# Kernel tuning notes

Hardware: AMD Instinct MI355X
Metric: run time of the kernel (lower is better)

Reference implementation:

```python
import jax, jax.numpy as jnp
import numpy as np

N_HEADS = 16


def setup_inputs() -> dict:
    key = jax.random.key(0)
    k1, k2, k3, k4, k5 = jax.random.split(key, 5)
    B, T, C = 2, 2048, 1024
    x = jax.random.normal(k1, (B, T, C), dtype=jnp.float32)
    rotary_cos_sin = jax.random.normal(k2, (T, C // N_HEADS), dtype=jnp.float32)  # unused by forward
    c = jax.random.normal(k3, (B, C), dtype=jnp.float32)  # unused by forward
    # Linear weights, torch convention: y = x @ W.T
    W_qkv = jax.random.normal(k4, (3 * C, C), dtype=jnp.float32) * (1.0 / np.sqrt(C))
    W_out = jax.random.normal(k5, (C, C), dtype=jnp.float32) * (1.0 / np.sqrt(C))
    return {"x": x, "rotary_cos_sin": rotary_cos_sin, "c": c, "W_qkv": W_qkv, "W_out": W_out}


def reference(x, rotary_cos_sin, c, W_qkv, W_out):
    B, T, C = x.shape
    H = N_HEADS
    D = C // H
    # qkv projection (no bias)
    qkv = jnp.einsum('btc,fc->btf', x, W_qkv)          # [B,T,3C]
    q, k, v = jnp.split(qkv, 3, axis=-1)
    q = q.reshape(B, T, H, D)
    k = k.reshape(B, T, H, D)
    v = v.reshape(B, T, H, D)
    # manual attention: full TxT score matrix, as in the original
    att = jnp.einsum('bthd,bshd->bhts', q, k) * (1.0 / jnp.sqrt(jnp.asarray(D, x.dtype)))
    att = jax.nn.softmax(att, axis=-1)
    # attn_dropout / resid_dropout are identity at inference
    y = jnp.einsum('bhts,bshd->bthd', att, v).reshape(B, T, C)
    return jnp.einsum('btc,oc->bto', y, W_out)
```

## Files before the change

kernel.cpp:

```cpp
#include <hip/hip_runtime.h>
#include <hip/hip_bf16.h>

typedef __bf16 bf16;
typedef __attribute__((ext_vector_type(4))) __bf16 bf16x4;
typedef __attribute__((ext_vector_type(8))) __bf16 bf16x8;
typedef __attribute__((ext_vector_type(4))) float f32x4;
typedef __attribute__((ext_vector_type(16))) float f32x16;

#define MFMA16(A, B, C) __builtin_amdgcn_mfma_f32_16x16x32_bf16((A), (B), (C), 0, 0, 0)
#define MFMA32(A, B, C) __builtin_amdgcn_mfma_f32_32x32x16_bf16((A), (B), (C), 0, 0, 0)

union U8 { unsigned w[4]; bf16x8 v; };

__device__ __forceinline__ void gload_lds16(const void* g, void* l) {
    __builtin_amdgcn_global_load_lds(
        (const __attribute__((address_space(1))) void*)g,
        (__attribute__((address_space(3))) void*)l,
        16, 0, 0);
}

__device__ __forceinline__ unsigned pk2(float a, float b) {
    union { bf16 h[2]; unsigned u; } t;
    t.h[0] = (bf16)a; t.h[1] = (bf16)b;
    return t.u;
}

__device__ __forceinline__ unsigned long long tr16(unsigned addr) {
    unsigned long long r;
    asm volatile("ds_read_b64_tr_b16 %0, %1" : "=v"(r) : "v"(addr));
    return r;
}

__global__ __launch_bounds__(256) void cast_f32_bf16(
    const float* __restrict__ in, bf16* __restrict__ out)
{
    const int i = (blockIdx.x * 256 + threadIdx.x) * 8;
    const float4 a = *(const float4*)(in + i);
    const float4 b = *(const float4*)(in + i + 4);
    bf16x8 o;
    o[0] = (bf16)a.x; o[1] = (bf16)a.y; o[2] = (bf16)a.z; o[3] = (bf16)a.w;
    o[4] = (bf16)b.x; o[5] = (bf16)b.y; o[6] = (bf16)b.z; o[7] = (bf16)b.w;
    *(bf16x8*)(out + i) = o;
}

template <typename OutT>
__global__ __launch_bounds__(256) void gemm_bt128(
    const bf16* __restrict__ A, const bf16* __restrict__ B, OutT* __restrict__ C,
    int M, int N, int K)
{
    constexpr int BK = 32;
    __shared__ __align__(16) bf16 sA[128 * BK];
    __shared__ __align__(16) bf16 sB[128 * BK];

    const int tid  = threadIdx.x;
    const int lane = tid & 63;
    const int wave = tid >> 6;
    const int wr   = wave >> 1;
    const int wc   = wave & 1;
    const int bm   = blockIdx.y * 128;
    const int bn   = blockIdx.x * 128;

    f32x4 acc[4][4] = {};

    const size_t ldb = (size_t)K * 2;
    const int srow = wave * 32 + (lane >> 2);
    const int scol = (lane & 3) * 16;
    const char* Ab = (const char*)A + (size_t)(bm + srow) * ldb + scol;
    const char* Bb = (const char*)B + (size_t)(bn + srow) * ldb + scol;
    char* ldsA = (char*)sA + wave * 2048;
    char* ldsB = (char*)sB + wave * 2048;

    const int arow = wr * 64 + (lane & 15);
    const int brow = wc * 64 + (lane & 15);
    const int koff = (lane >> 4) * 8;

    for (int k0 = 0; k0 < K; k0 += BK) {
        __syncthreads();
        const size_t kb = (size_t)k0 * 2;
        gload_lds16(Ab + kb,            ldsA);
        gload_lds16(Ab + kb + 16 * ldb, ldsA + 1024);
        gload_lds16(Bb + kb,            ldsB);
        gload_lds16(Bb + kb + 16 * ldb, ldsB + 1024);
        __syncthreads();

        bf16x8 af[4], bfr[4];
#pragma unroll
        for (int m = 0; m < 4; ++m)
            af[m] = *(const bf16x8*)&sA[(arow + m * 16) * BK + koff];
#pragma unroll
        for (int n = 0; n < 4; ++n)
            bfr[n] = *(const bf16x8*)&sB[(brow + n * 16) * BK + koff];
#pragma unroll
        for (int m = 0; m < 4; ++m)
#pragma unroll
            for (int n = 0; n < 4; ++n)
                acc[m][n] = MFMA16(af[m], bfr[n], acc[m][n]);
    }

    const int crow0 = bm + wr * 64 + (lane >> 4) * 4;
    const int ccol0 = bn + wc * 64 + (lane & 15);
#pragma unroll
    for (int m = 0; m < 4; ++m)
#pragma unroll
        for (int n = 0; n < 4; ++n)
#pragma unroll
            for (int j = 0; j < 4; ++j)
                C[(size_t)(crow0 + m * 16 + j) * N + ccol0 + n * 16] = (OutT)acc[m][n][j];
}

__global__ __launch_bounds__(512, 4) void attn32(
    const bf16* __restrict__ qkv, bf16* __restrict__ y)
{
    constexpr int T = 2048, F = 3072, Cd = 1024;
    constexpr float c1 = 0.18033688011112042f;

    __shared__ __align__(16) char smem[38912];

    const int tid = threadIdx.x, lane = tid & 63, w = tid >> 6;
    const int wq = w & 3, grp = w >> 2;
    const int hi = lane >> 5, q5 = lane & 31;
    const int bh = blockIdx.y, b = bh >> 4, h = bh & 15;
    const bf16* qkvb = qkv + (size_t)b * T * F;
    const int qcol = h * 64, kcol = Cd + h * 64, vcol = 2 * Cd + h * 64;

    char* sKg = smem + grp * 8192;
    char* sVg = smem + 16384 + grp * 8192;

    const int gq = blockIdx.x * 128 + wq * 32 + q5;
    bf16x8 qf[4];
#pragma unroll
    for (int s = 0; s < 4; ++s)
        qf[s] = *(const bf16x8*)(qkvb + (size_t)gq * F + qcol + s * 16 + hi * 8);

    const int ck0 = (wq * 2 + 0) * 64 + lane, ck1 = ck0 + 64;
    const int kvk0 = ck0 >> 3, d0k0 = ((ck0 & 7) ^ (kvk0 & 7)) << 3;
    const int kvk1 = ck1 >> 3, d0k1 = ((ck1 & 7) ^ (kvk1 & 7)) << 3;
    const int cv0 = ck0, cv1 = ck1;
    const int kvv0 = ((cv0 >> 1) & 3) | (((cv0 >> 5) & 1) << 2) | (((cv0 >> 4) & 1) << 3) | (((cv0 >> 6) & 3) << 4);
    const int dv0  = ((cv0 & 1) << 3) | (((cv0 >> 3) & 1) << 4) | (((cv0 >> 8) & 1) << 5);
    const int kvv1 = ((cv1 >> 1) & 3) | (((cv1 >> 5) & 1) << 2) | (((cv1 >> 4) & 1) << 3) | (((cv1 >> 6) & 3) << 4);
    const int dv1  = ((cv1 & 1) << 3) | (((cv1 >> 3) & 1) << 4) | (((cv1 >> 8) & 1) << 5);

    const size_t gbase = (size_t)grp * 1024 * F * 2;
    const char* kq0 = (const char*)qkvb + gbase + (size_t)(kvk0 * F + kcol + d0k0) * 2;
    const char* kq1 = (const char*)qkvb + gbase + (size_t)(kvk1 * F + kcol + d0k1) * 2;
    const char* vq0 = (const char*)qkvb + gbase + (size_t)(kvv0 * F + vcol + dv0) * 2;
    const char* vq1 = (const char*)qkvb + gbase + (size_t)(kvv1 * F + vcol + dv1) * 2;
    char* dstK0 = sKg + (wq * 2 + 0) * 1024;
    char* dstK1 = sKg + (wq * 2 + 1) * 1024;
    char* dstV0 = sVg + (wq * 2 + 0) * 1024;
    char* dstV1 = sVg + (wq * 2 + 1) * 1024;

    const unsigned sVoff = (unsigned)(uintptr_t)(__attribute__((address_space(3))) char*)(void*)sVg;
    const unsigned trb = sVoff + 8u * (unsigned)lane;
    const unsigned swz = (unsigned)(q5 & 7) << 4;

    f32x16 oacc[2] = {};
    float m_run = -3e38f, l_run = 0.f;

    for (int it = 0; it < 16; ++it) {
        __syncthreads();
        const size_t sb = (size_t)it * 64 * F * 2;
        gload_lds16(kq0 + sb, dstK0);
        gload_lds16(kq1 + sb, dstK1);
        gload_lds16(vq0 + sb, dstV0);
        gload_lds16(vq1 + sb, dstV1);
        __syncthreads();

        f32x16 sacc[2];
        __builtin_amdgcn_s_setprio(1);
#pragma unroll
        for (int a = 0; a < 2; ++a) {
            f32x16 acc = {};
#pragma unroll
            for (int dsl = 0; dsl < 4; ++dsl) {
                const unsigned cbyte = ((unsigned)(dsl * 32 + hi * 16)) ^ swz;
                bf16x8 kf = *(const bf16x8*)(sKg + (a * 32 + q5) * 128 + cbyte);
                acc = MFMA32(kf, qf[dsl], acc);
            }
            sacc[a] = acc;
        }
        __builtin_amdgcn_s_setprio(0);

        float mt = -3e38f;
#pragma unroll
        for (int a = 0; a < 2; ++a)
#pragma unroll
            for (int r = 0; r < 16; ++r) mt = fmaxf(mt, sacc[a][r]);
        mt = fmaxf(mt, __shfl_xor(mt, 32));
        if (__any(mt > m_run + 64.0f)) {
            const float mn = fmaxf(m_run, mt);
            const float al = __builtin_exp2f((m_run - mn) * c1);
            m_run = mn;
            l_run *= al;
#pragma unroll
            for (int d = 0; d < 2; ++d)
#pragma unroll
                for (int r = 0; r < 16; ++r) oacc[d][r] *= al;
        }
        const float mc = m_run * c1;

        float rs = 0.f;
        unsigned W[2][4][2];
#pragma unroll
        for (int a = 0; a < 2; ++a)
#pragma unroll
            for (int bb = 0; bb < 4; ++bb) {
                const float p0 = __builtin_exp2f(fmaf(sacc[a][4 * bb + 0], c1, -mc));
                const float p1 = __builtin_exp2f(fmaf(sacc[a][4 * bb + 1], c1, -mc));
                const float p2 = __builtin_exp2f(fmaf(sacc[a][4 * bb + 2], c1, -mc));
                const float p3 = __builtin_exp2f(fmaf(sacc[a][4 * bb + 3], c1, -mc));
                rs += (p0 + p1) + (p2 + p3);
                W[a][bb][0] = pk2(p0, p1);
                W[a][bb][1] = pk2(p2, p3);
            }
        l_run += rs;

        unsigned Zz[2][2][2];
#pragma unroll
        for (int a = 0; a < 2; ++a)
#pragma unroll
            for (int c = 0; c < 2; ++c)
#pragma unroll
                for (int ww = 0; ww < 2; ++ww) {
                    const unsigned yv = hi ? W[a][2 * c][ww] : W[a][2 * c + 1][ww];
                    Zz[a][c][ww] = (unsigned)__shfl_xor((int)yv, 32);
                }
        bf16x8 pb[4];
#pragma unroll
        for (int a = 0; a < 2; ++a)
#pragma unroll
            for (int c = 0; c < 2; ++c) {
                U8 u;
                u.w[0] = hi ? Zz[a][c][0] : W[a][2 * c][0];
                u.w[1] = hi ? Zz[a][c][1] : W[a][2 * c][1];
                u.w[2] = hi ? W[a][2 * c + 1][0] : Zz[a][c][0];
                u.w[3] = hi ? W[a][2 * c + 1][1] : Zz[a][c][1];
                pb[2 * a + c] = u.v;
            }

        unsigned long long t0[8], t1[8];
#pragma unroll
        for (int ks = 0; ks < 4; ++ks) {
            t0[2 * ks + 0] = tr16(trb + (unsigned)(ks * 1024));
            t0[2 * ks + 1] = tr16(trb + (unsigned)(ks * 1024 + 512));
        }
#pragma unroll
        for (int ks = 0; ks < 4; ++ks) {
            t1[2 * ks + 0] = tr16(trb + (unsigned)(4096 + ks * 1024));
            t1[2 * ks + 1] = tr16(trb + (unsigned)(4096 + ks * 1024 + 512));
        }
        asm volatile("s_waitcnt lgkmcnt(8)" ::: "memory");
        __builtin_amdgcn_sched_barrier(0);
        __builtin_amdgcn_s_setprio(1);
#pragma unroll
        for (int ks = 0; ks < 4; ++ks) {
            U8 u;
            u.w[0] = (unsigned)t0[2 * ks];     u.w[1] = (unsigned)(t0[2 * ks] >> 32);
            u.w[2] = (unsigned)t0[2 * ks + 1]; u.w[3] = (unsigned)(t0[2 * ks + 1] >> 32);
            oacc[0] = MFMA32(u.v, pb[ks], oacc[0]);
        }
        __builtin_amdgcn_s_setprio(0);
        asm volatile("s_waitcnt lgkmcnt(0)" ::: "memory");
        __builtin_amdgcn_sched_barrier(0);
        __builtin_amdgcn_s_setprio(1);
#pragma unroll
        for (int ks = 0; ks < 4; ++ks) {
            U8 u;
            u.w[0] = (unsigned)t1[2 * ks];     u.w[1] = (unsigned)(t1[2 * ks] >> 32);
            u.w[2] = (unsigned)t1[2 * ks + 1]; u.w[3] = (unsigned)(t1[2 * ks + 1] >> 32);
            oacc[1] = MFMA32(u.v, pb[ks], oacc[1]);
        }
        __builtin_amdgcn_s_setprio(0);
    }

    __syncthreads();
    float* Obuf  = (float*)smem;
    float* mlbuf = (float*)(smem + 36864);
    if (grp == 1) {
        float* po = Obuf + (wq * 64 + lane) * 36;
#pragma unroll
        for (int d5 = 0; d5 < 2; ++d5)
#pragma unroll
            for (int j = 0; j < 4; ++j) {
                f32x4 t;
                t[0] = oacc[d5][4 * j + 0]; t[1] = oacc[d5][4 * j + 1];
                t[2] = oacc[d5][4 * j + 2]; t[3] = oacc[d5][4 * j + 3];
                *(f32x4*)(po + d5 * 16 + 4 * j) = t;
            }
        mlbuf[(wq * 64 + lane) * 2 + 0] = m_run;
        mlbuf[(wq * 64 + lane) * 2 + 1] = l_run;
    }
    __syncthreads();
    if (grp == 0) {
        const float mB = mlbuf[(wq * 64 + lane) * 2 + 0];
        const float lB = mlbuf[(wq * 64 + lane) * 2 + 1];
        const float m  = fmaxf(m_run, mB);
        const float fA = __builtin_exp2f((m_run - m) * c1);
        const float fB = __builtin_exp2f((mB - m) * c1);
        const float lh = l_run * fA + lB * fB;
        const float lt = lh + __shfl_xor(lh, 32);
        const float inv = 1.f / lt;
        const float* po = Obuf + (wq * 64 + lane) * 36;
        bf16* yrow = y + (size_t)(b * T + gq) * Cd + h * 64;
#pragma unroll
        for (int d5 = 0; d5 < 2; ++d5)
#pragma unroll
            for (int bb = 0; bb < 4; ++bb) {
                const f32x4 ob = *(const f32x4*)(po + d5 * 16 + 4 * bb);
                bf16x4 o4;
#pragma unroll
                for (int jj = 0; jj < 4; ++jj)
                    o4[jj] = (bf16)((oacc[d5][4 * bb + jj] * fA + ob[jj] * fB) * inv);
                *(bf16x4*)(yrow + d5 * 32 + 8 * bb + 4 * hi) = o4;
            }
    }
}

extern "C" void kernel_launch(void* const* d_in, const int* in_sizes, int n_in,
                              void* d_out, int out_size, void* d_ws, size_t ws_size,
                              hipStream_t stream) {
    (void)in_sizes; (void)n_in; (void)out_size; (void)ws_size;
    const float* x    = (const float*)d_in[0];
    const float* Wqkv = (const float*)d_in[3];
    const float* Wout = (const float*)d_in[4];
    float* out = (float*)d_out;

    bf16* xb    = (bf16*)d_ws;
    bf16* wqkvb = xb    + (size_t)4096 * 1024;
    bf16* woutb = wqkvb + (size_t)3072 * 1024;
    bf16* qkv   = woutb + (size_t)1024 * 1024;
    bf16* yb    = qkv   + (size_t)4096 * 3072;

    cast_f32_bf16<<<4096 * 1024 / 2048, 256, 0, stream>>>(x, xb);
    cast_f32_bf16<<<3072 * 1024 / 2048, 256, 0, stream>>>(Wqkv, wqkvb);
    cast_f32_bf16<<<1024 * 1024 / 2048, 256, 0, stream>>>(Wout, woutb);

    gemm_bt128<bf16><<<dim3(3072 / 128, 4096 / 128), 256, 0, stream>>>(xb, wqkvb, qkv, 4096, 3072, 1024);
    attn32<<<dim3(2048 / 128, 2 * 16), 512, 0, stream>>>(qkv, yb);
    gemm_bt128<float><<<dim3(1024 / 128, 4096 / 128), 256, 0, stream>>>(yb, woutb, out, 4096, 1024, 1024);
}
```

Baseline: 226.4 us.

## Double-buffer K/V tiles in attention, fuse casts, narrow output GEMM tile

The attention kernel now double-buffers its K/V LDS tiles, issuing the next tile's global-to-LDS loads before computing on the current one. This removes the second barrier per iteration and is meant to hide load latency. The three f32-to-bf16 cast launches become one kernel, and the output projection GEMM uses 128x64 tiles so twice as many blocks run on a grid of only 256. LDS per attention block rises to 64KB, which may lower occupancy below the launch-bounds target.

```diff
diff --git a/kernel.cpp b/kernel.cpp
--- a/kernel.cpp
+++ b/kernel.cpp
@@ -31,26 +31,33 @@
     return r;
 }
 
-__global__ __launch_bounds__(256) void cast_f32_bf16(
-    const float* __restrict__ in, bf16* __restrict__ out)
+__global__ __launch_bounds__(256) void cast3_f32_bf16(
+    const float* __restrict__ x, const float* __restrict__ wq,
+    const float* __restrict__ wo, bf16* __restrict__ out)
 {
     const int i = (blockIdx.x * 256 + threadIdx.x) * 8;
-    const float4 a = *(const float4*)(in + i);
-    const float4 b = *(const float4*)(in + i + 4);
+    const float* src;
+    int off;
+    if (i < 4194304)      { src = x;  off = i; }
+    else if (i < 7340032) { src = wq; off = i - 4194304; }
+    else                  { src = wo; off = i - 7340032; }
+    const float4 a = *(const float4*)(src + off);
+    const float4 b = *(const float4*)(src + off + 4);
     bf16x8 o;
     o[0] = (bf16)a.x; o[1] = (bf16)a.y; o[2] = (bf16)a.z; o[3] = (bf16)a.w;
     o[4] = (bf16)b.x; o[5] = (bf16)b.y; o[6] = (bf16)b.z; o[7] = (bf16)b.w;
     *(bf16x8*)(out + i) = o;
 }
 
-template <typename OutT>
-__global__ __launch_bounds__(256) void gemm_bt128(
+template <typename OutT, int BN>
+__global__ __launch_bounds__(256) void gemm_bt(
     const bf16* __restrict__ A, const bf16* __restrict__ B, OutT* __restrict__ C,
     int M, int N, int K)
 {
     constexpr int BK = 32;
+    constexpr int NF = BN / 32;
     __shared__ __align__(16) bf16 sA[128 * BK];
-    __shared__ __align__(16) bf16 sB[128 * BK];
+    __shared__ __align__(16) bf16 sB[BN * BK];
 
     const int tid  = threadIdx.x;
     const int lane = tid & 63;
@@ -58,20 +65,28 @@
     const int wr   = wave >> 1;
     const int wc   = wave & 1;
     const int bm   = blockIdx.y * 128;
-    const int bn   = blockIdx.x * 128;
-
-    f32x4 acc[4][4] = {};
+    const int bn   = blockIdx.x * BN;
+
+    f32x4 acc[4][NF] = {};
 
     const size_t ldb = (size_t)K * 2;
-    const int srow = wave * 32 + (lane >> 2);
-    const int scol = (lane & 3) * 16;
-    const char* Ab = (const char*)A + (size_t)(bm + srow) * ldb + scol;
-    const char* Bb = (const char*)B + (size_t)(bn + srow) * ldb + scol;
+    const int srowA = wave * 32 + (lane >> 2);
+    const int scolA = (lane & 3) * 16;
+    const char* Ab = (const char*)A + (size_t)(bm + srowA) * ldb + scolA;
     char* ldsA = (char*)sA + wave * 2048;
-    char* ldsB = (char*)sB + wave * 2048;
+
+    const char* Bb;
+    char* ldsB;
+    if constexpr (BN == 128) {
+        Bb   = (const char*)B + (size_t)(bn + srowA) * ldb + scolA;
+        ldsB = (char*)sB + wave * 2048;
+    } else {
+        Bb   = (const char*)B + (size_t)(bn + (tid >> 2)) * ldb + (tid & 3) * 16;
+        ldsB = (char*)sB + tid * 16;
+    }
 
     const int arow = wr * 64 + (lane & 15);
-    const int brow = wc * 64 + (lane & 15);
+    const int brow = wc * (BN / 2) + (lane & 15);
     const int koff = (lane >> 4) * 8;
 
     for (int k0 = 0; k0 < K; k0 += BK) {
@@ -79,30 +94,34 @@
         const size_t kb = (size_t)k0 * 2;
         gload_lds16(Ab + kb,            ldsA);
         gload_lds16(Ab + kb + 16 * ldb, ldsA + 1024);
-        gload_lds16(Bb + kb,            ldsB);
-        gload_lds16(Bb + kb + 16 * ldb, ldsB + 1024);
+        if constexpr (BN == 128) {
+            gload_lds16(Bb + kb,            ldsB);
+            gload_lds16(Bb + kb + 16 * ldb, ldsB + 1024);
+        } else {
+            gload_lds16(Bb + kb, ldsB);
+        }
         __syncthreads();
 
-        bf16x8 af[4], bfr[4];
+        bf16x8 af[4], bfr[NF];
 #pragma unroll
         for (int m = 0; m < 4; ++m)
             af[m] = *(const bf16x8*)&sA[(arow + m * 16) * BK + koff];
 #pragma unroll
-        for (int n = 0; n < 4; ++n)
+        for (int n = 0; n < NF; ++n)
             bfr[n] = *(const bf16x8*)&sB[(brow + n * 16) * BK + koff];
 #pragma unroll
         for (int m = 0; m < 4; ++m)
 #pragma unroll
-            for (int n = 0; n < 4; ++n)
+            for (int n = 0; n < NF; ++n)
                 acc[m][n] = MFMA16(af[m], bfr[n], acc[m][n]);
     }
 
     const int crow0 = bm + wr * 64 + (lane >> 4) * 4;
-    const int ccol0 = bn + wc * 64 + (lane & 15);
+    const int ccol0 = bn + wc * (BN / 2) + (lane & 15);
 #pragma unroll
     for (int m = 0; m < 4; ++m)
 #pragma unroll
-        for (int n = 0; n < 4; ++n)
+        for (int n = 0; n < NF; ++n)
 #pragma unroll
             for (int j = 0; j < 4; ++j)
                 C[(size_t)(crow0 + m * 16 + j) * N + ccol0 + n * 16] = (OutT)acc[m][n][j];
@@ -114,7 +133,7 @@
     constexpr int T = 2048, F = 3072, Cd = 1024;
     constexpr float c1 = 0.18033688011112042f;
 
-    __shared__ __align__(16) char smem[38912];
+    __shared__ __align__(16) char smem[65536];
 
     const int tid = threadIdx.x, lane = tid & 63, w = tid >> 6;
     const int wq = w & 3, grp = w >> 2;
@@ -123,8 +142,7 @@
     const bf16* qkvb = qkv + (size_t)b * T * F;
     const int qcol = h * 64, kcol = Cd + h * 64, vcol = 2 * Cd + h * 64;
 
-    char* sKg = smem + grp * 8192;
-    char* sVg = smem + 16384 + grp * 8192;
+    const int grpbase = grp * 32768;
 
     const int gq = blockIdx.x * 128 + wq * 32 + q5;
     bf16x8 qf[4];
@@ -146,26 +164,39 @@
     const char* kq1 = (const char*)qkvb + gbase + (size_t)(kvk1 * F + kcol + d0k1) * 2;
     const char* vq0 = (const char*)qkvb + gbase + (size_t)(kvv0 * F + vcol + dv0) * 2;
     const char* vq1 = (const char*)qkvb + gbase + (size_t)(kvv1 * F + vcol + dv1) * 2;
-    char* dstK0 = sKg + (wq * 2 + 0) * 1024;
-    char* dstK1 = sKg + (wq * 2 + 1) * 1024;
-    char* dstV0 = sVg + (wq * 2 + 0) * 1024;
-    char* dstV1 = sVg + (wq * 2 + 1) * 1024;
-
-    const unsigned sVoff = (unsigned)(uintptr_t)(__attribute__((address_space(3))) char*)(void*)sVg;
-    const unsigned trb = sVoff + 8u * (unsigned)lane;
+
+    const unsigned smemAddr = (unsigned)(uintptr_t)(__attribute__((address_space(3))) char*)(void*)smem;
+    const unsigned trb0 = smemAddr + grpbase + 16384u + 8u * (unsigned)lane;
     const unsigned swz = (unsigned)(q5 & 7) << 4;
 
     f32x16 oacc[2] = {};
     float m_run = -3e38f, l_run = 0.f;
 
+    {
+        char* kb = smem + grpbase;
+        char* vb = smem + grpbase + 16384;
+        gload_lds16(kq0, kb + (wq * 2 + 0) * 1024);
+        gload_lds16(kq1, kb + (wq * 2 + 1) * 1024);
+        gload_lds16(vq0, vb + (wq * 2 + 0) * 1024);
+        gload_lds16(vq1, vb + (wq * 2 + 1) * 1024);
+    }
+
+    int cur = 0;
     for (int it = 0; it < 16; ++it) {
         __syncthreads();
-        const size_t sb = (size_t)it * 64 * F * 2;
-        gload_lds16(kq0 + sb, dstK0);
-        gload_lds16(kq1 + sb, dstK1);
-        gload_lds16(vq0 + sb, dstV0);
-        gload_lds16(vq1 + sb, dstV1);
-        __syncthreads();
+
+        if (it < 15) {
+            const size_t sb = (size_t)(it + 1) * 64 * F * 2;
+            char* kb = smem + grpbase + ((cur ^ 1) << 13);
+            char* vb = smem + grpbase + 16384 + ((cur ^ 1) << 13);
+            gload_lds16(kq0 + sb, kb + (wq * 2 + 0) * 1024);
+            gload_lds16(kq1 + sb, kb + (wq * 2 + 1) * 1024);
+            gload_lds16(vq0 + sb, vb + (wq * 2 + 0) * 1024);
+            gload_lds16(vq1 + sb, vb + (wq * 2 + 1) * 1024);
+        }
+
+        const char* sKc = smem + grpbase + (cur << 13);
+        const unsigned trbc = trb0 + (unsigned)(cur << 13);
 
         f32x16 sacc[2];
         __builtin_amdgcn_s_setprio(1);
@@ -175,7 +206,7 @@
 #pragma unroll
             for (int dsl = 0; dsl < 4; ++dsl) {
                 const unsigned cbyte = ((unsigned)(dsl * 32 + hi * 16)) ^ swz;
-                bf16x8 kf = *(const bf16x8*)(sKg + (a * 32 + q5) * 128 + cbyte);
+                bf16x8 kf = *(const bf16x8*)(sKc + (a * 32 + q5) * 128 + cbyte);
                 acc = MFMA32(kf, qf[dsl], acc);
             }
             sacc[a] = acc;
@@ -242,13 +273,13 @@
         unsigned long long t0[8], t1[8];
 #pragma unroll
         for (int ks = 0; ks < 4; ++ks) {
-            t0[2 * ks + 0] = tr16(trb + (unsigned)(ks * 1024));
-            t0[2 * ks + 1] = tr16(trb + (unsigned)(ks * 1024 + 512));
+            t0[2 * ks + 0] = tr16(trbc + (unsigned)(ks * 1024));
+            t0[2 * ks + 1] = tr16(trbc + (unsigned)(ks * 1024 + 512));
         }
 #pragma unroll
         for (int ks = 0; ks < 4; ++ks) {
-            t1[2 * ks + 0] = tr16(trb + (unsigned)(4096 + ks * 1024));
-            t1[2 * ks + 1] = tr16(trb + (unsigned)(4096 + ks * 1024 + 512));
+            t1[2 * ks + 0] = tr16(trbc + (unsigned)(4096 + ks * 1024));
+            t1[2 * ks + 1] = tr16(trbc + (unsigned)(4096 + ks * 1024 + 512));
         }
         asm volatile("s_waitcnt lgkmcnt(8)" ::: "memory");
         __builtin_amdgcn_sched_barrier(0);
@@ -272,6 +303,8 @@
             oacc[1] = MFMA32(u.v, pb[ks], oacc[1]);
         }
         __builtin_amdgcn_s_setprio(0);
+
+        cur ^= 1;
     }
 
     __syncthreads();
@@ -332,11 +365,9 @@
     bf16* qkv   = woutb + (size_t)1024 * 1024;
     bf16* yb    = qkv   + (size_t)4096 * 3072;
 
-    cast_f32_bf16<<<4096 * 1024 / 2048, 256, 0, stream>>>(x, xb);
-    cast_f32_bf16<<<3072 * 1024 / 2048, 256, 0, stream>>>(Wqkv, wqkvb);
-    cast_f32_bf16<<<1024 * 1024 / 2048, 256, 0, stream>>>(Wout, woutb);
-
-    gemm_bt128<bf16><<<dim3(3072 / 128, 4096 / 128), 256, 0, stream>>>(xb, wqkvb, qkv, 4096, 3072, 1024);
+    cast3_f32_bf16<<<8388608 / 2048, 256, 0, stream>>>(x, Wqkv, Wout, xb);
+
+    gemm_bt<bf16, 128><<<dim3(3072 / 128, 4096 / 128), 256, 0, stream>>>(xb, wqkvb, qkv, 4096, 3072, 1024);
     attn32<<<dim3(2048 / 128, 2 * 16), 512, 0, stream>>>(qkv, yb);
-    gemm_bt128<float><<<dim3(1024 / 128, 4096 / 128), 256, 0, stream>>>(yb, woutb, out, 4096, 1024, 1024);
-}
+    gemm_bt<float, 64><<<dim3(1024 / 64, 4096 / 128), 256, 0, stream>>>(yb, woutb, out, 4096, 1024, 1024);
+}
```

Result: faster. 209.0 us (-7.7%).
